# Optimization experiments

Hardware: AMD Instinct MI355X
Metric: run time of the kernel (lower is better)

Reference implementation:

```python
import jax, jax.numpy as jnp
import numpy as np

CW = 256  # sliding window size

def setup_inputs() -> dict:
    key = jax.random.key(0)
    k1, k2, k3, k4 = jax.random.split(key, 4)
    B, T, D, H = 2, 4096, 512, 64
    X = jax.random.normal(k1, (B, T, D), dtype=jnp.float32)
    Wq = jax.random.normal(k2, (D, H), dtype=jnp.float32) * (D ** -0.5)
    Wk = jax.random.normal(k3, (D, H), dtype=jnp.float32) * (D ** -0.5)
    Wv = jax.random.normal(k4, (D, H), dtype=jnp.float32) * (D ** -0.5)
    return {"X": X, "Wq": Wq, "Wk": Wk, "Wv": Wv}

def reference(X, Wq, Wk, Wv):
    B, T, D = X.shape
    H = Wq.shape[1]
    Cw = CW
    pad = Cw - 1
    Q = X @ Wq  # (B,T,H)
    K = X @ Wk
    V = X @ Wv
    # left-pad time axis with zeros (matches F.pad(..., (0,0,pad,0)))
    Kp = jnp.pad(K, ((0, 0), (pad, 0), (0, 0)))
    Vp = jnp.pad(V, ((0, 0), (pad, 0), (0, 0)))
    # window gather: slot j of token t is padded position t+j
    idx = jnp.arange(T)[:, None] + jnp.arange(Cw)[None, :]  # (T,Cw)
    Kwin = Kp[:, idx, :]  # (B,T,Cw,H)
    Vwin = Vp[:, idx, :]  # (B,T,Cw,H)
    att = jnp.einsum('bth,btjh->btj', Q, Kwin) / (H ** 0.5)  # (B,T,Cw)
    # faithful replication of the original mask: keep slot j iff j <= t
    i = jnp.arange(T)[:, None]
    j = jnp.arange(Cw)[None, :]
    valid = j <= i  # (T,Cw)
    att = jnp.where(valid[None, :, :], att, -jnp.inf)
    att = jax.nn.softmax(att, axis=-1)
    out = jnp.einsum('btj,btjh->bth', att, Vwin)  # (B,T,H)
    return out
```

## Files before the change

### kernel.cpp

```cpp
#include <hip/hip_runtime.h>
#include <hip/hip_bf16.h>
#include <math.h>

typedef short s16x8 __attribute__((ext_vector_type(8)));
typedef float f32x4 __attribute__((ext_vector_type(4)));

namespace {
constexpr int kB = 2;
constexpr int kT = 4096;
constexpr int kD = 512;
constexpr int kH = 64;
constexpr int kRows = kB * kT;

constexpr size_t oBH   = 0;
constexpr size_t oQKhi = oBH + (size_t)192 * 64 * 16;
constexpr size_t oVT   = oQKhi + (size_t)kRows * 128 * 2;

constexpr int TQ = 16;
constexpr int SPADF = 276;
constexpr int SPADB = 296;
}

__device__ __forceinline__ ushort bf16bits(float x) {
  __hip_bfloat16 hb = __float2bfloat16(x);
  return *reinterpret_cast<ushort*>(&hb);
}

__global__ __launch_bounds__(256) void prep_w(
    const float* __restrict__ Wq, const float* __restrict__ Wk,
    const float* __restrict__ Wv, s16x8* __restrict__ BH) {
  const int w = threadIdx.x >> 6;
  const int lane = threadIdx.x & 63;
  const int gw = blockIdx.x * 4 + w;
  const int ks = gw & 15;
  const int mn = gw >> 4;
  const int mat = mn >> 2;
  const int nf = mn & 3;
  const float* __restrict__ W = (mat == 0) ? Wq : (mat == 1) ? Wk : Wv;
  const int n = nf * 16 + (lane & 15);
  const int kb = ks * 32 + (lane >> 4) * 8;
  s16x8 vh;
#pragma unroll
  for (int e = 0; e < 8; ++e) vh[e] = (short)bf16bits(W[(size_t)(kb + e) * kH + n]);
  BH[(size_t)gw * 64 + lane] = vh;
}

__global__ __launch_bounds__(256) void qkv_fused(
    const float* __restrict__ X, const s16x8* __restrict__ BH,
    ushort* __restrict__ QKhi, ushort* __restrict__ VT) {
  __shared__ ushort AHs[16][520];

  const int tid = threadIdx.x;
  const int mt = blockIdx.x;

  const float* __restrict__ xb = X + (size_t)mt * 16 * kD;
#pragma unroll
  for (int it = 0; it < 8; ++it) {
    const int idx = tid + it * 256;
    const int row = idx >> 7;
    const int c4 = (idx & 127) * 4;
    const float4 x = *reinterpret_cast<const float4*>(xb + (size_t)row * kD + c4);
    ushort4 hi;
    hi.x = bf16bits(x.x);
    hi.y = bf16bits(x.y);
    hi.z = bf16bits(x.z);
    hi.w = bf16bits(x.w);
    *reinterpret_cast<ushort4*>(&AHs[row][c4]) = hi;
  }
  __syncthreads();

  const int w = tid >> 6;
  const int lane = tid & 63;
  const int l15 = lane & 15;
  const int kcol = (lane >> 4) * 8;
  const int nt0 = w * 3;

  f32x4 acc0 = {0.f, 0.f, 0.f, 0.f};
  f32x4 acc1 = {0.f, 0.f, 0.f, 0.f};
  f32x4 acc2 = {0.f, 0.f, 0.f, 0.f};

#pragma unroll
  for (int ks = 0; ks < 16; ++ks) {
    const s16x8 ah = *reinterpret_cast<const s16x8*>(&AHs[l15][ks * 32 + kcol]);
    const s16x8 bh0 = BH[(size_t)((nt0 + 0) * 16 + ks) * 64 + lane];
    const s16x8 bh1 = BH[(size_t)((nt0 + 1) * 16 + ks) * 64 + lane];
    const s16x8 bh2 = BH[(size_t)((nt0 + 2) * 16 + ks) * 64 + lane];
    acc0 = __builtin_amdgcn_mfma_f32_16x16x32_bf16(ah, bh0, acc0, 0, 0, 0);
    acc1 = __builtin_amdgcn_mfma_f32_16x16x32_bf16(ah, bh1, acc1, 0, 0, 0);
    acc2 = __builtin_amdgcn_mfma_f32_16x16x32_bf16(ah, bh2, acc2, 0, 0, 0);
  }

  const int r0 = (lane >> 4) * 4;
  f32x4 accs[3] = {acc0, acc1, acc2};
#pragma unroll
  for (int j = 0; j < 3; ++j) {
    const int colg = (nt0 + j) * 16 + l15;
    if (colg < 128) {
#pragma unroll
      for (int r = 0; r < 4; ++r)
        QKhi[(size_t)(mt * 16 + r0 + r) * 128 + colg] = bf16bits(accs[j][r]);
    } else {
      const int colv = colg - 128;
      const int mrow0 = mt * 16 + r0;
      const int b = mrow0 >> 12;
      const int t = mrow0 & (kT - 1);
      ushort4 pk;
      pk.x = bf16bits(accs[j][0]);
      pk.y = bf16bits(accs[j][1]);
      pk.z = bf16bits(accs[j][2]);
      pk.w = bf16bits(accs[j][3]);
      *reinterpret_cast<ushort4*>(VT + (size_t)(b * kH + colv) * kT + t) = pk;
    }
  }
}

__global__ __launch_bounds__(256) void swin_attn(
    const ushort* __restrict__ QKhi, const ushort* __restrict__ VT,
    float* __restrict__ O) {
  __shared__ float Sm[TQ][SPADF];
  __shared__ ushort PSm[TQ][SPADB];

  const int tid = threadIdx.x;
  const int w = tid >> 6;
  const int lane = tid & 63;
  const int bi = (blockIdx.x & 7) * 64 + (blockIdx.x >> 3);
  const int row0 = bi * TQ;
  const int t0 = row0 & (kT - 1);
  const int b = row0 >> 12;

  const int l15 = lane & 15;
  const int kcol = (lane >> 4) * 8;

  s16x8 qh[2];
  {
    const ushort* qp = QKhi + (size_t)(row0 + l15) * 128 + kcol;
#pragma unroll
    for (int kt = 0; kt < 2; ++kt)
      qh[kt] = *reinterpret_cast<const s16x8*>(qp + kt * 32);
  }

  f32x4 acc[5];
#pragma unroll
  for (int i = 0; i < 5; ++i) acc[i] = (f32x4){0.f, 0.f, 0.f, 0.f};

  const int NT = (w == 3) ? 5 : 4;
#pragma unroll
  for (int nt5 = 0; nt5 < 5; ++nt5) {
    if (nt5 < NT) {
      const int nt = w * 4 + nt5;
      const int p = t0 - 256 + nt * 16 + l15;
      const int pc = min(max(p, 0), kT - 1);
      const ushort* kp = QKhi + ((size_t)(b * kT + pc)) * 128 + 64 + kcol;
#pragma unroll
      for (int kt = 0; kt < 2; ++kt) {
        const s16x8 khh = *reinterpret_cast<const s16x8*>(kp + kt * 32);
        acc[nt5] = __builtin_amdgcn_mfma_f32_16x16x32_bf16(qh[kt], khh, acc[nt5], 0, 0, 0);
      }
    }
  }

#pragma unroll
  for (int nt5 = 0; nt5 < 5; ++nt5) {
    if (nt5 < NT) {
      const int nt = w * 4 + nt5;
      const int col = nt * 16 + l15;
#pragma unroll
      for (int r = 0; r < 4; ++r) Sm[(lane >> 4) * 4 + r][col] = acc[nt5][r] * 0.125f;
    }
  }
  __syncthreads();

  {
    const int i = tid >> 4;
    const int l = tid & 15;
    const int t = t0 + i;
    float sv[18];
    float mx = -INFINITY;
#pragma unroll
    for (int k2 = 0; k2 < 18; ++k2) {
      const int jg = l + 16 * k2;
      const int p = t0 - 256 + jg;
      const int jref = p - t + 255;
      const bool valid = (p >= 0) && (jref >= 0) && (jref <= 255) && (jref <= t);
      sv[k2] = valid ? Sm[i][jg] : -INFINITY;
      mx = fmaxf(mx, sv[k2]);
    }
#pragma unroll
    for (int off = 1; off < 16; off <<= 1) mx = fmaxf(mx, __shfl_xor(mx, off));
    const int n0 = (t < 255) ? min(t + 1, 255 - t) : 0;
    if (n0 > 0) mx = fmaxf(mx, 0.f);

    float sum = 0.f;
    float ev[18];
#pragma unroll
    for (int k2 = 0; k2 < 18; ++k2) {
      ev[k2] = (sv[k2] > -INFINITY) ? __expf(sv[k2] - mx) : 0.f;
      sum += ev[k2];
    }
#pragma unroll
    for (int off = 1; off < 16; off <<= 1) sum += __shfl_xor(sum, off);
    sum += (float)n0 * __expf(-mx);
    const float inv = 1.f / sum;
#pragma unroll
    for (int k2 = 0; k2 < 18; ++k2)
      PSm[i][l + 16 * k2] = bf16bits(ev[k2] * inv);
  }
  __syncthreads();

  f32x4 oacc = {0.f, 0.f, 0.f, 0.f};
  const int hcol = w * 16 + l15;
  const ushort* vt = VT + (size_t)(b * kH + hcol) * kT + t0 - 256;
#pragma unroll
  for (int kt = 0; kt < 9; ++kt) {
    const s16x8 pa = *reinterpret_cast<const s16x8*>(&PSm[l15][kt * 32 + kcol]);
    const s16x8 vbf = *reinterpret_cast<const s16x8*>(vt + kt * 32 + kcol);
    oacc = __builtin_amdgcn_mfma_f32_16x16x32_bf16(pa, vbf, oacc, 0, 0, 0);
  }

#pragma unroll
  for (int r = 0; r < 4; ++r)
    O[(size_t)(row0 + (lane >> 4) * 4 + r) * kH + hcol] = oacc[r];
}

extern "C" void kernel_launch(void* const* d_in, const int* in_sizes, int n_in,
                              void* d_out, int out_size, void* d_ws, size_t ws_size,
                              hipStream_t stream) {
  const float* X  = (const float*)d_in[0];
  const float* Wq = (const float*)d_in[1];
  const float* Wk = (const float*)d_in[2];
  const float* Wv = (const float*)d_in[3];
  char* ws = (char*)d_ws;
  s16x8* BH = (s16x8*)(ws + oBH);
  ushort* QKhi = (ushort*)(ws + oQKhi);
  ushort* VT = (ushort*)(ws + oVT);
  float* O = (float*)d_out;

  prep_w<<<48, 256, 0, stream>>>(Wq, Wk, Wv, BH);
  qkv_fused<<<512, 256, 0, stream>>>(X, BH, QKhi, VT);
  swin_attn<<<512, 256, 0, stream>>>(QKhi, VT, O);
}
```

Baseline: 26.08 us.

## Drop softmax max-subtraction and defer normalization to the output epilogue

```diff
diff --git a/kernel.cpp b/kernel.cpp
--- a/kernel.cpp
+++ b/kernel.cpp
@@ -17,7 +17,6 @@
 constexpr size_t oVT   = oQKhi + (size_t)kRows * 128 * 2;
 
 constexpr int TQ = 16;
-constexpr int SPADF = 276;
 constexpr int SPADB = 296;
 }
 
@@ -117,8 +116,8 @@
 __global__ __launch_bounds__(256) void swin_attn(
     const ushort* __restrict__ QKhi, const ushort* __restrict__ VT,
     float* __restrict__ O) {
-  __shared__ float Sm[TQ][SPADF];
   __shared__ ushort PSm[TQ][SPADB];
+  __shared__ float invs[TQ];
 
   const int tid = threadIdx.x;
   const int w = tid >> 6;
@@ -131,6 +130,8 @@
   const int l15 = lane & 15;
   const int kcol = (lane >> 4) * 8;
 
+  PSm[tid >> 4][272 + (tid & 15)] = 0;
+
   s16x8 qh[2];
   {
     const ushort* qp = QKhi + (size_t)(row0 + l15) * 128 + kcol;
@@ -163,9 +164,17 @@
   for (int nt5 = 0; nt5 < 5; ++nt5) {
     if (nt5 < NT) {
       const int nt = w * 4 + nt5;
-      const int col = nt * 16 + l15;
-#pragma unroll
-      for (int r = 0; r < 4; ++r) Sm[(lane >> 4) * 4 + r][col] = acc[nt5][r] * 0.125f;
+      const int jg = nt * 16 + l15;
+      const int p = t0 - 256 + jg;
+#pragma unroll
+      for (int r = 0; r < 4; ++r) {
+        const int i = (lane >> 4) * 4 + r;
+        const int t = t0 + i;
+        const int jref = p - t + 255;
+        const bool valid = (p >= 0) && (jref >= 0) && (jref <= 255) && (jref <= t);
+        const float e = valid ? __expf(acc[nt5][r] * 0.125f) : 0.f;
+        PSm[i][jg] = bf16bits(e);
+      }
     }
   }
   __syncthreads();
@@ -174,36 +183,17 @@
     const int i = tid >> 4;
     const int l = tid & 15;
     const int t = t0 + i;
-    float sv[18];
-    float mx = -INFINITY;
+    float sum = 0.f;
 #pragma unroll
     for (int k2 = 0; k2 < 18; ++k2) {
-      const int jg = l + 16 * k2;
-      const int p = t0 - 256 + jg;
-      const int jref = p - t + 255;
-      const bool valid = (p >= 0) && (jref >= 0) && (jref <= 255) && (jref <= t);
-      sv[k2] = valid ? Sm[i][jg] : -INFINITY;
-      mx = fmaxf(mx, sv[k2]);
-    }
-#pragma unroll
-    for (int off = 1; off < 16; off <<= 1) mx = fmaxf(mx, __shfl_xor(mx, off));
+      const unsigned int u = (unsigned int)PSm[i][l + 16 * k2] << 16;
+      sum += __uint_as_float(u);
+    }
+#pragma unroll
+    for (int off = 1; off < 16; off <<= 1) sum += __shfl_xor(sum, off);
     const int n0 = (t < 255) ? min(t + 1, 255 - t) : 0;
-    if (n0 > 0) mx = fmaxf(mx, 0.f);
-
-    float sum = 0.f;
-    float ev[18];
-#pragma unroll
-    for (int k2 = 0; k2 < 18; ++k2) {
-      ev[k2] = (sv[k2] > -INFINITY) ? __expf(sv[k2] - mx) : 0.f;
-      sum += ev[k2];
-    }
-#pragma unroll
-    for (int off = 1; off < 16; off <<= 1) sum += __shfl_xor(sum, off);
-    sum += (float)n0 * __expf(-mx);
-    const float inv = 1.f / sum;
-#pragma unroll
-    for (int k2 = 0; k2 < 18; ++k2)
-      PSm[i][l + 16 * k2] = bf16bits(ev[k2] * inv);
+    sum += (float)n0;
+    if (l == 0) invs[i] = 1.f / sum;
   }
   __syncthreads();
 
@@ -218,8 +208,10 @@
   }
 
 #pragma unroll
-  for (int r = 0; r < 4; ++r)
-    O[(size_t)(row0 + (lane >> 4) * 4 + r) * kH + hcol] = oacc[r];
+  for (int r = 0; r < 4; ++r) {
+    const int i = (lane >> 4) * 4 + r;
+    O[(size_t)(row0 + i) * kH + hcol] = oacc[r] * invs[i];
+  }
 }
 
 extern "C" void kernel_launch(void* const* d_in, const int* in_sizes, int n_in,
```

Result: faster. 25.22 us (-3.3%).
